# Kernel tuning notes

Measured on AMD Instinct MI355X. Metric: run time of the kernel, lower is better.

## Reference

```python
import math
import jax, jax.numpy as jnp
import numpy as np

NUM_FREQ = 10  # NeRF-style L=10 -> enc dim 3 + 3*2*10 = 63

def pos_encode(coords):
    # freq_bands = 2^i * pi, i = 0..L-1
    freq = (2.0 ** jnp.arange(NUM_FREQ, dtype=coords.dtype)) * math.pi
    scaled = coords[..., None] * freq                      # [E, 3, L]
    enc = jnp.stack([jnp.sin(scaled), jnp.cos(scaled)], axis=-1)  # [E, 3, L, 2]
    enc = enc.reshape(coords.shape[0], -1)                 # [E, 60] interleaved sin/cos
    return jnp.concatenate([coords, enc], axis=-1)         # [E, 63]

def setup_inputs() -> dict:
    key = jax.random.key(0)
    ks = jax.random.split(key, 9)
    N, M, K, C = 65536, 16384, 32, 64
    E = M * K
    x = jax.random.normal(ks[0], (N, C), jnp.float32)
    pos = jax.random.normal(ks[1], (N, 3), jnp.float32)
    batch = jnp.sort(jax.random.randint(ks[2], (N,), 0, 8))
    idx = jax.random.randint(ks[3], (M,), 0, N)
    row = jnp.sort(jax.random.randint(ks[4], (E,), 0, M))
    col = jax.random.randint(ks[5], (E,), 0, N)
    d_in = C + 3 + 3 * 2 * NUM_FREQ  # 127
    def lin(k, i, o):
        s = 1.0 / np.sqrt(i)
        kw, kb = jax.random.split(k)
        return (jax.random.uniform(kw, (i, o), jnp.float32, -s, s),
                jax.random.uniform(kb, (o,), jnp.float32, -s, s))
    lw1, lb1 = lin(ks[6], d_in, 128)
    lw2, lb2 = lin(ks[7], 128, 128)
    gw, gb = lin(ks[8], 128, 256)
    return dict(x=x, pos=pos, batch=batch, idx=idx, row=row, col=col,
                lw1=lw1, lb1=lb1, lw2=lw2, lb2=lb2, gw=gw, gb=gb)

def reference(x, pos, batch, idx, row, col, lw1, lb1, lw2, lb2, gw, gb):
    M = idx.shape[0]
    pos_idx = pos[idx]                         # [M, 3] sampled centers
    pos_diff = pos[col] - pos_idx[row]         # [E, 3] neighbor offsets
    pe = pos_encode(pos_diff)                  # [E, 63]
    edge_in = jnp.concatenate([x[col], pe], axis=-1)   # [E, 127]
    # local_nn: Linear->ReLU->Linear (no final activation, per MLP_Wrapper)
    h = jax.nn.relu(edge_in @ lw1 + lb1)       # [E, 128]
    edge_feat = h @ lw2 + lb2                  # [E, 128]
    # scatter_reduce amax, include_self=False: empty rows stay 0
    agg = jax.ops.segment_max(edge_feat, row, num_segments=M)
    agg = jnp.where(jnp.isneginf(agg), jnp.zeros((), agg.dtype), agg)
    out = agg @ gw + gb                        # [M, 256] global_nn (single Linear)
    return out, pos_idx, batch[idx]
```

## Files before the change

kernel.cpp:

```cpp
#include <hip/hip_runtime.h>
#include <math.h>

#define NN 65536
#define MM 16384
#define EE 524288
#define CF 64
#define HD 128
#define OD 256
#define RPB 16
#define PITCH 129

typedef __bf16 bf16x8 __attribute__((ext_vector_type(8)));
typedef __bf16 bf16x4 __attribute__((ext_vector_type(4)));
typedef float f32x4 __attribute__((ext_vector_type(4)));

__device__ __forceinline__ unsigned enc_f(float f) {
    unsigned u = __float_as_uint(f);
    return (u & 0x80000000u) ? ~u : (u | 0x80000000u);
}
__device__ __forceinline__ float dec_f(unsigned e) {
    unsigned u = (e & 0x80000000u) ? (e ^ 0x80000000u) : ~e;
    return __uint_as_float(u);
}
#define ENC_NEG_INF 0x007FFFFFu

__device__ __forceinline__ unsigned bf_bits(float f) {
    __bf16 b = (__bf16)f;
    return (unsigned)__builtin_bit_cast(unsigned short, b);
}

#define WS_FRAG_OFF 0
#define WS_ROWPTR_OFF 65536
#define WS_XBF_OFF 131072
#define WS_PD_OFF (131072 + 8388608)

__global__ void k_pre(__bf16* __restrict__ fragbuf, int* __restrict__ rowptr,
                      __bf16* __restrict__ xbf, float4* __restrict__ pdbuf,
                      const float* __restrict__ lw1, const float* __restrict__ lw2,
                      const float* __restrict__ x, const int* __restrict__ row,
                      const int* __restrict__ col,
                      const float* __restrict__ pos, const int* __restrict__ batch,
                      const int* __restrict__ idx, float* __restrict__ out) {
    const int b = blockIdx.x;
    const int t = threadIdx.x;
    if (b == 0) {
        const int lane = t & 63;
        const int wv = t >> 6;
        const int q = lane >> 4;
        const int ln = lane & 15;
        #pragma unroll
        for (int fi = 0; fi < 16; ++fi) {
            const int nt = (fi >> 2) & 1, kk = fi & 3;
            const int n = wv * 32 + nt * 16 + ln;
            bf16x8 f;
            #pragma unroll
            for (int j = 0; j < 8; ++j) {
                const int c = kk * 32 + q * 8 + j;
                const int rk = (c < 67) ? c : c - 1;
                f[j] = (fi < 8) ? (__bf16)((c == 67) ? 0.0f : lw1[rk * HD + n])
                                : (__bf16)lw2[c * HD + n];
            }
            *(bf16x8*)&fragbuf[((size_t)fi * 256 + t) * 8] = f;
        }
    } else if (b <= 65) {
        const int i = (b - 1) * 256 + t;
        if (i <= MM) {
            int lo = 0, hi = EE;
            while (lo < hi) { int mid = (lo + hi) >> 1; if (row[mid] < i) lo = mid + 1; else hi = mid; }
            rowptr[i] = lo;
        }
    } else if (b <= 129) {
        const int m = (b - 66) * 256 + t;
        if (m < MM) {
            const int s = idx[m];
            out[MM * OD + m * 3 + 0] = pos[s * 3 + 0];
            out[MM * OD + m * 3 + 1] = pos[s * 3 + 1];
            out[MM * OD + m * 3 + 2] = pos[s * 3 + 2];
            out[MM * OD + MM * 3 + m] = (float)batch[s];
        }
    } else if (b <= 1153) {
        const size_t base = ((size_t)(b - 130) * 256 + t) * 16;
        const float4* xs = (const float4*)(x + base);
        const float4 a = xs[0], c = xs[1], d = xs[2], e = xs[3];
        bf16x8 o0, o1;
        o0[0] = (__bf16)a.x; o0[1] = (__bf16)a.y; o0[2] = (__bf16)a.z; o0[3] = (__bf16)a.w;
        o0[4] = (__bf16)c.x; o0[5] = (__bf16)c.y; o0[6] = (__bf16)c.z; o0[7] = (__bf16)c.w;
        o1[0] = (__bf16)d.x; o1[1] = (__bf16)d.y; o1[2] = (__bf16)d.z; o1[3] = (__bf16)d.w;
        o1[4] = (__bf16)e.x; o1[5] = (__bf16)e.y; o1[6] = (__bf16)e.z; o1[7] = (__bf16)e.w;
        *(bf16x8*)&xbf[base] = o0;
        *(bf16x8*)&xbf[base + 8] = o1;
    } else {
        const int e = (b - 1154) * 256 + t;
        const int r = row[e];
        const int c = col[e];
        const int s = idx[r];
        float4 pd;
        pd.x = pos[c * 3 + 0] - pos[s * 3 + 0];
        pd.y = pos[c * 3 + 1] - pos[s * 3 + 1];
        pd.z = pos[c * 3 + 2] - pos[s * 3 + 2];
        pd.w = 0.0f;
        pdbuf[e] = pd;
    }
}

__launch_bounds__(256, 3)
__global__ void k_fused(const __bf16* __restrict__ xbf, const float4* __restrict__ pdbuf,
                        const int* __restrict__ row, const int* __restrict__ col,
                        const int* __restrict__ rowptr, const __bf16* __restrict__ fragbuf,
                        const float* __restrict__ lb1, const float* __restrict__ lb2,
                        const float* __restrict__ gw, const float* __restrict__ gb,
                        float* __restrict__ out) {
    __shared__ __align__(16) __bf16 einX[64][64];
    __shared__ __align__(16) __bf16 einP[64][64];
    __shared__ __align__(16) __bf16 hbuf[64][HD];
    __shared__ unsigned maxbuf[(RPB + 1) * PITCH];
    __shared__ int srow[2][64];
    const int t = threadIdx.x;
    const int lane = t & 63;
    const int wv = t >> 6;
    const int q = lane >> 4;
    const int ln = lane & 15;
    const int lsw = ln & 7;
    const int m0 = blockIdx.x * RPB;

    const int es = rowptr[m0];
    const int ee = rowptr[m0 + RPB];
    const int ntiles = (ee - es + 63) >> 6;

    for (int i = t; i < (RPB + 1) * PITCH; i += 256) maxbuf[i] = ENC_NEG_INF;

    const int pe_e = t >> 2, pe_part = t & 3, pe_esw = pe_e & 7;
    bf16x8 s0, s1;
    auto issue = [&](int tt) {
        const int eg = min(es + tt * 64 + pe_e, EE - 1);
        const int c = col[eg];
        const bf16x8* xr = (const bf16x8*)(xbf + (size_t)c * CF) + pe_part * 2;
        s0 = xr[0]; s1 = xr[1];
    };
    auto commit = [&]() {
        *(bf16x8*)&einX[pe_e][((pe_part * 2 + 0) ^ pe_esw) * 8] = s0;
        *(bf16x8*)&einX[pe_e][((pe_part * 2 + 1) ^ pe_esw) * 8] = s1;
    };
    auto do_pe = [&](int tt) {
        if (t < 192) {
            const int e = t & 63, d = t >> 6;
            const int sb = tt & 1;
            const int eidx = es + tt * 64 + e;
            const int eg = min(eidx, EE - 1);
            const int esw = e & 7;
            const float4 P = pdbuf[eg];
            const float pd = (d == 0) ? P.x : ((d == 1) ? P.y : P.z);
            if (d == 0) {
                srow[sb][e] = (eidx < ee) ? (row[eg] - m0) : RPB;
                uint2 pkt;
                pkt.x = bf_bits(P.x) | (bf_bits(P.y) << 16);
                pkt.y = bf_bits(P.z);
                *(uint2*)&einP[e][esw * 8] = pkt;
            }
            const float fr = __builtin_amdgcn_fractf(pd * 0.5f);
            float sv = __builtin_amdgcn_sinf(fr);
            float cv = __builtin_amdgcn_cosf(fr);
            #pragma unroll
            for (int l = 0; l < 10; ++l) {
                const int jP = 4 + d * 20 + l * 2;
                *(unsigned*)&einP[e][((jP >> 3) ^ esw) * 8 + (jP & 7)] =
                    bf_bits(sv) | (bf_bits(cv) << 16);
                const float s2 = 2.0f * sv * cv;
                const float c2 = 1.0f - 2.0f * sv * sv;
                sv = s2; cv = c2;
            }
        }
    };

    float4 b1q[2];
    #pragma unroll
    for (int nt = 0; nt < 2; ++nt)
        b1q[nt] = *(const float4*)&lb1[wv * 32 + nt * 16 + q * 4];

    if (ntiles > 0) {
        issue(0);
        commit();
        do_pe(0);
        if (ntiles > 1) issue(1);
    }
    __syncthreads();

    for (int tt = 0; tt < ntiles; ++tt) {
        {
            bf16x8 w1f[2][4];
            #pragma unroll
            for (int nt = 0; nt < 2; ++nt)
                #pragma unroll
                for (int kk = 0; kk < 4; ++kk)
                    w1f[nt][kk] = *(const bf16x8*)&fragbuf[((size_t)(nt * 4 + kk) * 256 + t) * 8];

            f32x4 acc[2][4];
            #pragma unroll
            for (int nt = 0; nt < 2; ++nt)
                #pragma unroll
                for (int et = 0; et < 4; ++et)
                    acc[nt][et] = (f32x4){b1q[nt].x, b1q[nt].y, b1q[nt].z, b1q[nt].w};
            #pragma unroll
            for (int et = 0; et < 4; ++et) {
                const int e = et * 16 + ln;
                bf16x8 a[4];
                a[0] = *(const bf16x8*)&einX[e][(q ^ lsw) * 8];
                a[1] = *(const bf16x8*)&einX[e][((4 + q) ^ lsw) * 8];
                a[2] = *(const bf16x8*)&einP[e][(q ^ lsw) * 8];
                a[3] = *(const bf16x8*)&einP[e][((4 + q) ^ lsw) * 8];
                #pragma unroll
                for (int kk = 0; kk < 4; ++kk) {
                    acc[0][et] = __builtin_amdgcn_mfma_f32_16x16x32_bf16(w1f[0][kk], a[kk], acc[0][et], 0, 0, 0);
                    acc[1][et] = __builtin_amdgcn_mfma_f32_16x16x32_bf16(w1f[1][kk], a[kk], acc[1][et], 0, 0, 0);
                }
            }
            #pragma unroll
            for (int et = 0; et < 4; ++et) {
                const int e = et * 16 + ln;
                #pragma unroll
                for (int nt = 0; nt < 2; ++nt) {
                    bf16x4 hv;
                    hv[0] = (__bf16)fmaxf(acc[nt][et][0], 0.0f);
                    hv[1] = (__bf16)fmaxf(acc[nt][et][1], 0.0f);
                    hv[2] = (__bf16)fmaxf(acc[nt][et][2], 0.0f);
                    hv[3] = (__bf16)fmaxf(acc[nt][et][3], 0.0f);
                    const int chunk = wv * 4 + nt * 2 + (q >> 1);
                    *(bf16x4*)&hbuf[e][((chunk ^ lsw) * 8) + (q & 1) * 4] = hv;
                }
            }
        }
        __syncthreads();

        {
            if (tt + 1 < ntiles) { commit(); issue(tt + 2 < ntiles ? tt + 2 : tt + 1); }
            bf16x8 w2f[2][4];
            #pragma unroll
            for (int nt = 0; nt < 2; ++nt)
                #pragma unroll
                for (int kk = 0; kk < 4; ++kk)
                    w2f[nt][kk] = *(const bf16x8*)&fragbuf[((size_t)(8 + nt * 4 + kk) * 256 + t) * 8];

            f32x4 acc2[4][2];
            #pragma unroll
            for (int nt = 0; nt < 2; ++nt) {
                const float b2 = lb2[wv * 32 + nt * 16 + ln];
                #pragma unroll
                for (int et = 0; et < 4; ++et)
                    acc2[et][nt] = (f32x4){b2, b2, b2, b2};
            }
            #pragma unroll
            for (int et = 0; et < 4; ++et) {
                const int e = et * 16 + ln;
                #pragma unroll
                for (int kk = 0; kk < 4; ++kk) {
                    bf16x8 ah = *(const bf16x8*)&hbuf[e][((kk * 4 + q) ^ lsw) * 8];
                    acc2[et][0] = __builtin_amdgcn_mfma_f32_16x16x32_bf16(ah, w2f[0][kk], acc2[et][0], 0, 0, 0);
                    acc2[et][1] = __builtin_amdgcn_mfma_f32_16x16x32_bf16(ah, w2f[1][kk], acc2[et][1], 0, 0, 0);
                }
            }
            if (tt + 1 < ntiles) do_pe(tt + 1);
            const int sb = tt & 1;
            #pragma unroll
            for (int et = 0; et < 4; ++et) {
                const int4 R = *(const int4*)&srow[sb][et * 16 + q * 4];
                #pragma unroll
                for (int nt = 0; nt < 2; ++nt) {
                    unsigned* base = maxbuf + (wv * 32 + nt * 16 + ln);
                    const f32x4 vv = acc2[et][nt];
                    int cur = R.x;
                    float m = vv[0];
                    if (R.y != cur) { atomicMax(base + cur * PITCH, enc_f(m)); cur = R.y; m = vv[1]; }
                    else m = fmaxf(m, vv[1]);
                    if (R.z != cur) { atomicMax(base + cur * PITCH, enc_f(m)); cur = R.z; m = vv[2]; }
                    else m = fmaxf(m, vv[2]);
                    if (R.w != cur) { atomicMax(base + cur * PITCH, enc_f(m)); cur = R.w; m = vv[3]; }
                    else m = fmaxf(m, vv[3]);
                    atomicMax(base + cur * PITCH, enc_f(m));
                }
            }
        }
        __syncthreads();
    }

    float* afin = (float*)hbuf;
    for (int i = t; i < RPB * HD; i += 256) {
        const unsigned e = maxbuf[(i >> 7) * PITCH + (i & 127)];
        afin[i] = (e == ENC_NEG_INF) ? 0.0f : dec_f(e);
    }
    __syncthreads();

    const int j4 = (t & 63) * 4;
    const int rbase = (t >> 6) * 4;
    float facc[4][4];
    const float4 bias = *(const float4*)&gb[j4];
    #pragma unroll
    for (int r = 0; r < 4; ++r) { facc[r][0] = bias.x; facc[r][1] = bias.y; facc[r][2] = bias.z; facc[r][3] = bias.w; }
    for (int k = 0; k < 128; k += 4) {
        float4 w0 = *(const float4*)&gw[(k + 0) * OD + j4];
        float4 w1 = *(const float4*)&gw[(k + 1) * OD + j4];
        float4 w2 = *(const float4*)&gw[(k + 2) * OD + j4];
        float4 w3 = *(const float4*)&gw[(k + 3) * OD + j4];
        #pragma unroll
        for (int r = 0; r < 4; ++r) {
            float4 av = *(const float4*)&afin[(rbase + r) * HD + k];
            facc[r][0] += av.x * w0.x + av.y * w1.x + av.z * w2.x + av.w * w3.x;
            facc[r][1] += av.x * w0.y + av.y * w1.y + av.z * w2.y + av.w * w3.y;
            facc[r][2] += av.x * w0.z + av.y * w1.z + av.z * w2.z + av.w * w3.z;
            facc[r][3] += av.x * w0.w + av.y * w1.w + av.z * w2.w + av.w * w3.w;
        }
    }
    #pragma unroll
    for (int r = 0; r < 4; ++r) {
        float4 v; v.x = facc[r][0]; v.y = facc[r][1]; v.z = facc[r][2]; v.w = facc[r][3];
        *(float4*)&out[(size_t)(m0 + rbase + r) * OD + j4] = v;
    }
}

extern "C" void kernel_launch(void* const* d_in, const int* in_sizes, int n_in,
                              void* d_out, int out_size, void* d_ws, size_t ws_size,
                              hipStream_t stream) {
    const float* x   = (const float*)d_in[0];
    const float* pos = (const float*)d_in[1];
    const int* batch = (const int*)d_in[2];
    const int* idx   = (const int*)d_in[3];
    const int* row   = (const int*)d_in[4];
    const int* col   = (const int*)d_in[5];
    const float* lw1 = (const float*)d_in[6];
    const float* lb1 = (const float*)d_in[7];
    const float* lw2 = (const float*)d_in[8];
    const float* lb2 = (const float*)d_in[9];
    const float* gw  = (const float*)d_in[10];
    const float* gb  = (const float*)d_in[11];
    float* out = (float*)d_out;
    __bf16* fragbuf = (__bf16*)((char*)d_ws + WS_FRAG_OFF);
    int* rowptr     = (int*)((char*)d_ws + WS_ROWPTR_OFF);
    __bf16* xbf     = (__bf16*)((char*)d_ws + WS_XBF_OFF);
    float4* pdbuf   = (float4*)((char*)d_ws + WS_PD_OFF);

    hipLaunchKernelGGL(k_pre, dim3(1 + 65 + 64 + 1024 + 2048), dim3(256), 0, stream,
                       fragbuf, rowptr, xbf, pdbuf, lw1, lw2, x, row, col, pos, batch, idx, out);
    hipLaunchKernelGGL(k_fused, dim3(MM / RPB), dim3(256), 0, stream,
                       xbf, pdbuf, row, col, rowptr, fragbuf, lb1, lb2, gw, gb, out);
}
```

Before: 100.4 us.

## Precompute full positional encoding in pre-kernel and stream it into fused kernel

The sin/cos positional encoding moves out of the fused MLP kernel into the preprocessing kernel. There it is written as a 64-wide bf16 row per edge, staged through shared memory so the global stores are coalesced. The fused kernel then loads the encoded rows alongside the gathered x features in its issue/commit pipeline and only loads row indices separately. This removes transcendental and LDS-write work from the MFMA loop, at the cost of roughly 64 MB of extra global traffic (write plus read) versus the 8 MB float4 offset buffer.

```diff
diff --git a/kernel.cpp b/kernel.cpp
--- a/kernel.cpp
+++ b/kernel.cpp
@@ -32,10 +32,10 @@
 #define WS_FRAG_OFF 0
 #define WS_ROWPTR_OFF 65536
 #define WS_XBF_OFF 131072
-#define WS_PD_OFF (131072 + 8388608)
+#define WS_PE_OFF (131072 + 8388608)
 
 __global__ void k_pre(__bf16* __restrict__ fragbuf, int* __restrict__ rowptr,
-                      __bf16* __restrict__ xbf, float4* __restrict__ pdbuf,
+                      __bf16* __restrict__ xbf, __bf16* __restrict__ pebuf,
                       const float* __restrict__ lw1, const float* __restrict__ lw2,
                       const float* __restrict__ x, const int* __restrict__ row,
                       const int* __restrict__ col,
@@ -90,21 +90,42 @@
         *(bf16x8*)&xbf[base] = o0;
         *(bf16x8*)&xbf[base + 8] = o1;
     } else {
-        const int e = (b - 1154) * 256 + t;
+        __shared__ __align__(16) __bf16 pe_s[256][64];
+        const int e0 = (b - 1154) * 256;
+        const int e = e0 + t;
         const int r = row[e];
         const int c = col[e];
         const int s = idx[r];
-        float4 pd;
-        pd.x = pos[c * 3 + 0] - pos[s * 3 + 0];
-        pd.y = pos[c * 3 + 1] - pos[s * 3 + 1];
-        pd.z = pos[c * 3 + 2] - pos[s * 3 + 2];
-        pd.w = 0.0f;
-        pdbuf[e] = pd;
+        float pd[3];
+        #pragma unroll
+        for (int d = 0; d < 3; ++d) pd[d] = pos[c * 3 + d] - pos[s * 3 + d];
+        uint2 pk;
+        pk.x = bf_bits(pd[0]) | (bf_bits(pd[1]) << 16);
+        pk.y = bf_bits(pd[2]);
+        *(uint2*)&pe_s[t][0] = pk;
+        #pragma unroll
+        for (int d = 0; d < 3; ++d) {
+            const float fr0 = __builtin_amdgcn_fractf(pd[d] * 0.5f);
+            float sv = __builtin_amdgcn_sinf(fr0);
+            float cv = __builtin_amdgcn_cosf(fr0);
+            #pragma unroll
+            for (int l = 0; l < 10; ++l) {
+                *(unsigned*)&pe_s[t][4 + d * 20 + l * 2] = bf_bits(sv) | (bf_bits(cv) << 16);
+                const float s2 = 2.0f * sv * cv;
+                const float c2 = 1.0f - 2.0f * sv * sv;
+                sv = s2; cv = c2;
+            }
+        }
+        __syncthreads();
+        const uint4* src = (const uint4*)&pe_s[0][0];
+        uint4* dst = (uint4*)&pebuf[(size_t)e0 * 64];
+        #pragma unroll
+        for (int i = 0; i < 8; ++i) dst[i * 256 + t] = src[i * 256 + t];
     }
 }
 
 __launch_bounds__(256, 3)
-__global__ void k_fused(const __bf16* __restrict__ xbf, const float4* __restrict__ pdbuf,
+__global__ void k_fused(const __bf16* __restrict__ xbf, const __bf16* __restrict__ pebuf,
                         const int* __restrict__ row, const int* __restrict__ col,
                         const int* __restrict__ rowptr, const __bf16* __restrict__ fragbuf,
                         const float* __restrict__ lb1, const float* __restrict__ lb2,
@@ -130,45 +151,26 @@
     for (int i = t; i < (RPB + 1) * PITCH; i += 256) maxbuf[i] = ENC_NEG_INF;
 
     const int pe_e = t >> 2, pe_part = t & 3, pe_esw = pe_e & 7;
-    bf16x8 s0, s1;
+    bf16x8 s0, s1, p0, p1;
     auto issue = [&](int tt) {
         const int eg = min(es + tt * 64 + pe_e, EE - 1);
         const int c = col[eg];
         const bf16x8* xr = (const bf16x8*)(xbf + (size_t)c * CF) + pe_part * 2;
         s0 = xr[0]; s1 = xr[1];
+        const bf16x8* pr = (const bf16x8*)(pebuf + (size_t)eg * 64) + pe_part * 2;
+        p0 = pr[0]; p1 = pr[1];
     };
     auto commit = [&]() {
         *(bf16x8*)&einX[pe_e][((pe_part * 2 + 0) ^ pe_esw) * 8] = s0;
         *(bf16x8*)&einX[pe_e][((pe_part * 2 + 1) ^ pe_esw) * 8] = s1;
+        *(bf16x8*)&einP[pe_e][((pe_part * 2 + 0) ^ pe_esw) * 8] = p0;
+        *(bf16x8*)&einP[pe_e][((pe_part * 2 + 1) ^ pe_esw) * 8] = p1;
     };
-    auto do_pe = [&](int tt) {
-        if (t < 192) {
-            const int e = t & 63, d = t >> 6;
-            const int sb = tt & 1;
-            const int eidx = es + tt * 64 + e;
+    auto load_srow = [&](int tt) {
+        if (t < 64) {
+            const int eidx = es + tt * 64 + t;
             const int eg = min(eidx, EE - 1);
-            const int esw = e & 7;
-            const float4 P = pdbuf[eg];
-            const float pd = (d == 0) ? P.x : ((d == 1) ? P.y : P.z);
-            if (d == 0) {
-                srow[sb][e] = (eidx < ee) ? (row[eg] - m0) : RPB;
-                uint2 pkt;
-                pkt.x = bf_bits(P.x) | (bf_bits(P.y) << 16);
-                pkt.y = bf_bits(P.z);
-                *(uint2*)&einP[e][esw * 8] = pkt;
-            }
-            const float fr = __builtin_amdgcn_fractf(pd * 0.5f);
-            float sv = __builtin_amdgcn_sinf(fr);
-            float cv = __builtin_amdgcn_cosf(fr);
-            #pragma unroll
-            for (int l = 0; l < 10; ++l) {
-                const int jP = 4 + d * 20 + l * 2;
-                *(unsigned*)&einP[e][((jP >> 3) ^ esw) * 8 + (jP & 7)] =
-                    bf_bits(sv) | (bf_bits(cv) << 16);
-                const float s2 = 2.0f * sv * cv;
-                const float c2 = 1.0f - 2.0f * sv * sv;
-                sv = s2; cv = c2;
-            }
+            srow[tt & 1][t] = (eidx < ee) ? (row[eg] - m0) : RPB;
         }
     };
 
@@ -180,7 +182,7 @@
     if (ntiles > 0) {
         issue(0);
         commit();
-        do_pe(0);
+        load_srow(0);
         if (ntiles > 1) issue(1);
     }
     __syncthreads();
@@ -232,7 +234,11 @@
         __syncthreads();
 
         {
-            if (tt + 1 < ntiles) { commit(); issue(tt + 2 < ntiles ? tt + 2 : tt + 1); }
+            if (tt + 1 < ntiles) {
+                commit();
+                issue(tt + 2 < ntiles ? tt + 2 : tt + 1);
+                load_srow(tt + 1);
+            }
             bf16x8 w2f[2][4];
             #pragma unroll
             for (int nt = 0; nt < 2; ++nt)
@@ -258,7 +264,6 @@
                     acc2[et][1] = __builtin_amdgcn_mfma_f32_16x16x32_bf16(ah, w2f[1][kk], acc2[et][1], 0, 0, 0);
                 }
             }
-            if (tt + 1 < ntiles) do_pe(tt + 1);
             const int sb = tt & 1;
             #pragma unroll
             for (int et = 0; et < 4; ++et) {
@@ -335,10 +340,10 @@
     __bf16* fragbuf = (__bf16*)((char*)d_ws + WS_FRAG_OFF);
     int* rowptr     = (int*)((char*)d_ws + WS_ROWPTR_OFF);
     __bf16* xbf     = (__bf16*)((char*)d_ws + WS_XBF_OFF);
-    float4* pdbuf   = (float4*)((char*)d_ws + WS_PD_OFF);
+    __bf16* pebuf   = (__bf16*)((char*)d_ws + WS_PE_OFF);
 
     hipLaunchKernelGGL(k_pre, dim3(1 + 65 + 64 + 1024 + 2048), dim3(256), 0, stream,
-                       fragbuf, rowptr, xbf, pdbuf, lw1, lw2, x, row, col, pos, batch, idx, out);
+                       fragbuf, rowptr, xbf, pebuf, lw1, lw2, x, row, col, pos, batch, idx, out);
     hipLaunchKernelGGL(k_fused, dim3(MM / RPB), dim3(256), 0, stream,
-                       xbf, pdbuf, row, col, rowptr, fragbuf, lb1, lb2, gw, gb, out);
-}
+                       xbf, pebuf, row, col, rowptr, fragbuf, lb1, lb2, gw, gb, out);
+}
```

Result: slower. 105.8 us (+5.4%).
